# Kernel tuning notes

Measured on AMD Instinct MI355X. Metric: run time of the kernel, lower is better.

## Reference

```python
import jax, jax.numpy as jnp
import numpy as np


def setup_inputs() -> dict:
    key = jax.random.key(0)
    ks = jax.random.split(key, 8)
    T, B, I, H, A, R = 256, 256, 9, 1024, 4, 38
    return {
        "inputs": jax.random.normal(ks[0], (T, B, I), dtype=jnp.float32),
        "hidden0": jax.random.normal(ks[1], (B, H), dtype=jnp.float32),
        "actions": jax.random.normal(ks[2], (T, B, A), dtype=jnp.float32),
        "reward": jax.random.normal(ks[3], (B, R), dtype=jnp.float32),
        # parameters, initialized with the same scales as the torch module
        "i2h": jax.random.normal(ks[4], (I, H), dtype=jnp.float32) * float(10 * np.sqrt(2.0 / (I + H))),
        "h2h": jax.random.normal(ks[5], (H, H), dtype=jnp.float32) * float(np.sqrt(2.0 / H)),
        "a2h": jax.random.normal(ks[6], (A, H), dtype=jnp.float32) * float(np.sqrt(2.0 / (H + A))),
        "r2h": jax.random.normal(ks[7], (R, H), dtype=jnp.float32) * float(0.1 * np.sqrt(2.0 / (H + R))),
        "bh": jnp.zeros((1, H), dtype=jnp.float32),
        "r": 0.5 * jnp.ones((1, H), dtype=jnp.float32),  # inertia
        "k_action": 1,
    }


def reference(inputs, hidden0, actions, reward, i2h, h2h, a2h, r2h, bh, r, k_action):
    # reward @ r2h + bh is constant across timesteps -> hoist out of the scan
    rbias = reward @ r2h + bh  # [B, H]

    def step(hidden, xs):
        inp_t, act_t = xs  # [B, I], [B, A]
        h_cand = jnp.tanh(inp_t @ i2h + hidden @ h2h + k_action * (act_t @ a2h) + rbias)
        hidden = (1 - r) * h_cand + r * hidden  # leaky state blend
        return hidden, hidden

    _, hiddens = jax.lax.scan(step, hidden0, (inputs, actions))
    return hiddens  # [T, B, H] == list of hiddens in forward_sequence
```

## Files before the change

kernel.cpp:

```cpp
#include <hip/hip_runtime.h>
#include <stdint.h>
#include <math.h>

#define TT 256
#define BB 256
#define II 9
#define HH 1024
#define AAx 4
#define RR 38
#define BH (BB*HH)
#define NJB 16

typedef __attribute__((ext_vector_type(8))) short short8;
typedef __attribute__((ext_vector_type(4))) float f32x4;
typedef __attribute__((ext_vector_type(4))) unsigned int u32x4;

__device__ __forceinline__ float bf2f(unsigned short u){
  union{unsigned int i; float f;} v; v.i = ((unsigned int)u)<<16; return v.f;
}
__device__ __forceinline__ unsigned short f2bf(float f){
  union{float f; unsigned int i;} v; v.f = f;
  unsigned int r = (v.i + 0x7FFFu + ((v.i>>16)&1u)) >> 16;
  return (unsigned short)r;
}

#define ISSUE2(d0,d1,s0,s1)                                                   \
  asm volatile("global_load_dwordx4 %0, %2, off offset:" s0 " sc0 sc1\n\t"    \
               "global_load_dwordx4 %1, %2, off offset:" s1 " sc0 sc1"        \
               : "=&v"(d0), "=&v"(d1) : "v"(ap) : "memory")

#define WAITP(n,q0,q1)                                                        \
  asm volatile("s_waitcnt vmcnt(" n ")" : "+v"(q0), "+v"(q1) :: "memory")

#define STORE_CC(p,x)                                                         \
  asm volatile("global_store_dword %0, %1, off sc0 sc1" :: "v"(p), "v"(x) : "memory")

#define CVTPK(d,s0,s1)                                                        \
  asm("v_cvt_pk_bf16_f32 %0, %1, %2" : "=v"(d) : "v"(s0), "v"(s1))

__global__ __launch_bounds__(512, 2) void rnn_persist(
    const float* __restrict__ inp,  const float* __restrict__ hid0,
    const float* __restrict__ act,  const float* __restrict__ rew,
    const float* __restrict__ i2h,  const float* __restrict__ h2h,
    const float* __restrict__ a2h,  const float* __restrict__ r2h,
    const float* __restrict__ bh,   const float* __restrict__ rr,
    const int*   __restrict__ kact_p,
    float* __restrict__ out, int* __restrict__ cnt)
{
  __shared__ f32x4 part[8*4*64];
  __shared__ unsigned short sexth[16*32];
  __shared__ unsigned short sextl[16*32];

  const int tid   = threadIdx.x;
  const int w     = tid >> 6;
  const int l     = tid & 63;
  const int row16 = l & 15;
  const int quad  = l >> 4;
  const int g     = blockIdx.x & 15;
  const int jb    = blockIdx.x >> 4;

  const float kact = (float)kact_p[0];

  short8 wbh[4][4], wbl[4][4];
  #pragma unroll
  for (int ki=0; ki<4; ki++){
    const int kb = w*128 + ki*32 + quad*8;
    #pragma unroll
    for (int nt=0; nt<4; nt++){
      const int n = jb*64 + nt*16 + row16;
      short8 vh, vl;
      #pragma unroll
      for (int j=0; j<8; j++){
        const float bv = h2h[(size_t)(kb+j)*HH + n];
        const unsigned short hh = f2bf(bv);
        vh[j] = (short)hh;
        vl[j] = (short)f2bf(bv - bf2f(hh));
      }
      wbh[ki][nt] = vh; wbl[ki][nt] = vl;
    }
  }
  short8 webh[4], webl[4];
  #pragma unroll
  for (int nt=0; nt<4; nt++){
    short8 vh, vl;
    #pragma unroll
    for (int j=0; j<8; j++){
      const int k = quad*8 + j;
      const int n = jb*64 + nt*16 + row16;
      float bv = 0.f;
      if (w == 0){
        if (k < II)          bv = i2h[(size_t)k*HH + n];
        else if (k < II+AAx) bv = kact * a2h[(size_t)(k-II)*HH + n];
      }
      const unsigned short hh = f2bf(bv);
      vh[j] = (short)hh;
      vl[j] = (short)f2bf(bv - bf2f(hh));
    }
    webh[nt] = vh; webl[nt] = vl;
  }

  const int ecol = jb*64 + w*16 + row16;
  float r_own = 0.f, romr = 0.f;
  float h_own[4] = {0,0,0,0}, rb[4] = {0,0,0,0};
  if (w < 4){
    r_own = rr[ecol];
    romr  = 1.f - r_own;
    #pragma unroll
    for (int i=0; i<4; i++){
      const int br = 16*g + 4*quad + i;
      h_own[i] = hid0[(size_t)br*HH + ecol];
      float s = bh[ecol];
      for (int q=0; q<RR; q++) s += rew[(size_t)br*RR + q] * r2h[(size_t)q*HH + ecol];
      rb[i] = s;
    }
  }

  sexth[tid] = 0; sextl[tid] = 0;
  const int st_act = (tid < 16*13);
  const int st_row = st_act ? (tid / 13) : 0;
  const int st_q   = st_act ? (tid % 13) : 0;
  __syncthreads();

  float xv_cur = 0.f, xv_nxt = 0.f;
  if (st_act){
    const int br = 16*g + st_row;
    xv_cur = (st_q < II) ? inp[(size_t)br*II + st_q]
                         : act[(size_t)br*AAx + (st_q - II)];
  }

  const int arow = 16*g + row16;

  for (int t=0; t<TT; t++){
    if (st_act){
      const unsigned short hh = f2bf(xv_cur);
      sexth[st_row*32 + st_q] = hh;
      sextl[st_row*32 + st_q] = f2bf(xv_cur - bf2f(hh));
    }
    __syncthreads();

    const float* __restrict__ hp = t ? (out + (size_t)(t-1)*BH) : hid0;
    const float* ap = hp + (size_t)arow*HH + (size_t)w*128 + quad*8;

    f32x4 acc[4];
    #pragma unroll
    for (int nt=0; nt<4; nt++){ acc[nt].x=0.f; acc[nt].y=0.f; acc[nt].z=0.f; acc[nt].w=0.f; }

    auto doKi = [&](int ki, const f32x4& q0, const f32x4& q1){
      u32x4 ahw, alw;
      CVTPK(ahw[0], q0[0], q0[1]);
      CVTPK(ahw[1], q0[2], q0[3]);
      CVTPK(ahw[2], q1[0], q1[1]);
      CVTPK(ahw[3], q1[2], q1[3]);
      const float l0 = q0[0] - __builtin_bit_cast(float, ahw[0] << 16);
      const float l1 = q0[1] - __builtin_bit_cast(float, ahw[0] & 0xFFFF0000u);
      const float l2 = q0[2] - __builtin_bit_cast(float, ahw[1] << 16);
      const float l3 = q0[3] - __builtin_bit_cast(float, ahw[1] & 0xFFFF0000u);
      const float l4 = q1[0] - __builtin_bit_cast(float, ahw[2] << 16);
      const float l5 = q1[1] - __builtin_bit_cast(float, ahw[2] & 0xFFFF0000u);
      const float l6 = q1[2] - __builtin_bit_cast(float, ahw[3] << 16);
      const float l7 = q1[3] - __builtin_bit_cast(float, ahw[3] & 0xFFFF0000u);
      CVTPK(alw[0], l0, l1);
      CVTPK(alw[1], l2, l3);
      CVTPK(alw[2], l4, l5);
      CVTPK(alw[3], l6, l7);
      const short8 ah = __builtin_bit_cast(short8, ahw);
      const short8 al = __builtin_bit_cast(short8, alw);
      #pragma unroll
      for (int nt=0; nt<4; nt++){
        acc[nt] = __builtin_amdgcn_mfma_f32_16x16x32_bf16(ah, wbh[ki][nt], acc[nt], 0,0,0);
        acc[nt] = __builtin_amdgcn_mfma_f32_16x16x32_bf16(al, wbh[ki][nt], acc[nt], 0,0,0);
        acc[nt] = __builtin_amdgcn_mfma_f32_16x16x32_bf16(ah, wbl[ki][nt], acc[nt], 0,0,0);
      }
    };

    {
      f32x4 p0,p1,q0,q1;
      ISSUE2(p0,p1,"0","16");
      ISSUE2(q0,q1,"128","144");
      WAITP("2",p0,p1);
      doKi(0,p0,p1);
      ISSUE2(p0,p1,"256","272");
      WAITP("2",q0,q1);
      doKi(1,q0,q1);
      ISSUE2(q0,q1,"384","400");
      {
        const int tt2 = (t+1 < TT) ? (t+1) : (TT-1);
        const int br  = 16*g + st_row;
        const float* xp = st_act
          ? ((st_q < II) ? inp + ((size_t)tt2*BB + br)*II  + st_q
                         : act + ((size_t)tt2*BB + br)*AAx + (st_q - II))
          : inp;
        xv_nxt = *xp;
      }
      WAITP("3",p0,p1);
      doKi(2,p0,p1);
      WAITP("1",q0,q1);
      doKi(3,q0,q1);
    }

    if (w == 0){
      const short8 aeh = *(const short8*)&sexth[row16*32 + quad*8];
      const short8 ael = *(const short8*)&sextl[row16*32 + quad*8];
      #pragma unroll
      for (int nt=0; nt<4; nt++){
        acc[nt] = __builtin_amdgcn_mfma_f32_16x16x32_bf16(aeh, webh[nt], acc[nt], 0,0,0);
        acc[nt] = __builtin_amdgcn_mfma_f32_16x16x32_bf16(ael, webh[nt], acc[nt], 0,0,0);
        acc[nt] = __builtin_amdgcn_mfma_f32_16x16x32_bf16(aeh, webl[nt], acc[nt], 0,0,0);
      }
    }

    #pragma unroll
    for (int nt=0; nt<4; nt++) part[(w*4 + nt)*64 + l] = acc[nt];
    __syncthreads();

    if (w < 4){
      f32x4 z = part[(0*4 + w)*64 + l];
      #pragma unroll
      for (int s=1; s<8; s++){
        const f32x4 p = part[(s*4 + w)*64 + l];
        z.x += p.x; z.y += p.y; z.z += p.z; z.w += p.w;
      }
      const float zz[4] = {z.x, z.y, z.z, z.w};
      #pragma unroll
      for (int i=0; i<4; i++){
        const float x  = zz[i] + rb[i];
        const float hc = tanhf(x);
        const float hn = romr*hc + r_own*h_own[i];
        h_own[i] = hn;
        const int br = 16*g + 4*quad + i;
        float* op = out + (size_t)t*BH + (size_t)br*HH + ecol;
        STORE_CC(op, hn);
      }
    }

    asm volatile("s_waitcnt vmcnt(0)" ::: "memory");
    __syncthreads();
    if (tid == 0){
      __hip_atomic_fetch_add(&cnt[g*32], 1, __ATOMIC_RELAXED, __HIP_MEMORY_SCOPE_AGENT);
      const int target = NJB*(t+1);
      while (__hip_atomic_load(&cnt[g*32], __ATOMIC_RELAXED, __HIP_MEMORY_SCOPE_AGENT) < target)
        __builtin_amdgcn_s_sleep(1);
    }
    __syncthreads();

    xv_cur = xv_nxt;
  }
}

extern "C" void kernel_launch(void* const* d_in, const int* in_sizes, int n_in,
                              void* d_out, int out_size, void* d_ws, size_t ws_size,
                              hipStream_t stream) {
  const float* inp  = (const float*)d_in[0];
  const float* hid0 = (const float*)d_in[1];
  const float* act  = (const float*)d_in[2];
  const float* rew  = (const float*)d_in[3];
  const float* i2h  = (const float*)d_in[4];
  const float* h2h  = (const float*)d_in[5];
  const float* a2h  = (const float*)d_in[6];
  const float* r2h  = (const float*)d_in[7];
  const float* bh   = (const float*)d_in[8];
  const float* rr   = (const float*)d_in[9];
  const int*   kact = (const int*)d_in[10];
  float* out = (float*)d_out;

  int* cnt = (int*)d_ws;
  hipMemsetAsync(d_ws, 0, 4096, stream);

  rnn_persist<<<256, 512, 0, stream>>>(inp, hid0, act, rew, i2h, h2h, a2h, r2h,
                                       bh, rr, kact, out, cnt);
}
```

Before: 1.259 ms.

## Replace group atomic-counter barrier with per-block flags and per-wave polling

```diff
diff --git a/kernel.cpp b/kernel.cpp
--- a/kernel.cpp
+++ b/kernel.cpp
@@ -14,6 +14,7 @@
 typedef __attribute__((ext_vector_type(8))) short short8;
 typedef __attribute__((ext_vector_type(4))) float f32x4;
 typedef __attribute__((ext_vector_type(4))) unsigned int u32x4;
+typedef __attribute__((ext_vector_type(2))) unsigned int u32x2;
 
 __device__ __forceinline__ float bf2f(unsigned short u){
   union{unsigned int i; float f;} v; v.i = ((unsigned int)u)<<16; return v.f;
@@ -50,6 +51,9 @@
   __shared__ f32x4 part[8*4*64];
   __shared__ unsigned short sexth[16*32];
   __shared__ unsigned short sextl[16*32];
+  __shared__ short8 sweh[4*64];
+  __shared__ short8 swel[4*64];
+  __shared__ int done4[2];
 
   const int tid   = threadIdx.x;
   const int w     = tid >> 6;
@@ -79,24 +83,23 @@
       wbh[ki][nt] = vh; wbl[ki][nt] = vl;
     }
   }
-  short8 webh[4], webl[4];
-  #pragma unroll
-  for (int nt=0; nt<4; nt++){
-    short8 vh, vl;
-    #pragma unroll
-    for (int j=0; j<8; j++){
-      const int k = quad*8 + j;
-      const int n = jb*64 + nt*16 + row16;
-      float bv = 0.f;
-      if (w == 0){
+  if (w == 0){
+    #pragma unroll
+    for (int nt=0; nt<4; nt++){
+      short8 vh, vl;
+      #pragma unroll
+      for (int j=0; j<8; j++){
+        const int k = quad*8 + j;
+        const int n = jb*64 + nt*16 + row16;
+        float bv = 0.f;
         if (k < II)          bv = i2h[(size_t)k*HH + n];
         else if (k < II+AAx) bv = kact * a2h[(size_t)(k-II)*HH + n];
-      }
-      const unsigned short hh = f2bf(bv);
-      vh[j] = (short)hh;
-      vl[j] = (short)f2bf(bv - bf2f(hh));
-    }
-    webh[nt] = vh; webl[nt] = vl;
+        const unsigned short hh = f2bf(bv);
+        vh[j] = (short)hh;
+        vl[j] = (short)f2bf(bv - bf2f(hh));
+      }
+      sweh[nt*64 + l] = vh; swel[nt*64 + l] = vl;
+    }
   }
 
   const int ecol = jb*64 + w*16 + row16;
@@ -116,30 +119,42 @@
   }
 
   sexth[tid] = 0; sextl[tid] = 0;
+  if (tid < 2) done4[tid] = 0;
   const int st_act = (tid < 16*13);
   const int st_row = st_act ? (tid / 13) : 0;
   const int st_q   = st_act ? (tid % 13) : 0;
   __syncthreads();
 
-  float xv_cur = 0.f, xv_nxt = 0.f;
-  if (st_act){
+  const int arow = 16*g + row16;
+  unsigned* flown = (unsigned*)((char*)cnt + 1024 + (size_t)g*64 + (size_t)jb*4);
+  const unsigned* fp = (const unsigned*)((char*)cnt + 1024 + (size_t)g*64 + (size_t)w*8);
+
+  float xvr;
+  f32x4 L0a,L0b,L1a,L1b,L2a,L2b,L3a,L3b;
+  u32x2 fpre;
+  {
     const int br = 16*g + st_row;
-    xv_cur = (st_q < II) ? inp[(size_t)br*II + st_q]
-                         : act[(size_t)br*AAx + (st_q - II)];
-  }
-
-  const int arow = 16*g + row16;
+    const float* xp0 = st_act
+      ? ((st_q < II) ? inp + (size_t)br*II + st_q
+                     : act + (size_t)br*AAx + (st_q - II))
+      : inp;
+    asm volatile("global_load_dword %0, %1, off" : "=&v"(xvr) : "v"(xp0) : "memory");
+    const float* ap = hid0 + (size_t)arow*HH + (size_t)w*128 + quad*8;
+    ISSUE2(L0a,L0b,"0","16");
+    ISSUE2(L1a,L1b,"128","144");
+    ISSUE2(L2a,L2b,"256","272");
+    ISSUE2(L3a,L3b,"384","400");
+  }
 
   for (int t=0; t<TT; t++){
+    asm volatile("s_waitcnt vmcnt(8)" : "+v"(xvr) :: "memory");
     if (st_act){
-      const unsigned short hh = f2bf(xv_cur);
+      const unsigned short hh = f2bf(xvr);
       sexth[st_row*32 + st_q] = hh;
-      sextl[st_row*32 + st_q] = f2bf(xv_cur - bf2f(hh));
-    }
-    __syncthreads();
-
-    const float* __restrict__ hp = t ? (out + (size_t)(t-1)*BH) : hid0;
-    const float* ap = hp + (size_t)arow*HH + (size_t)w*128 + quad*8;
+      sextl[st_row*32 + st_q] = f2bf(xvr - bf2f(hh));
+    }
+    asm volatile("s_waitcnt lgkmcnt(0)" ::: "memory");
+    __builtin_amdgcn_s_barrier();
 
     f32x4 acc[4];
     #pragma unroll
@@ -173,45 +188,32 @@
       }
     };
 
-    {
-      f32x4 p0,p1,q0,q1;
-      ISSUE2(p0,p1,"0","16");
-      ISSUE2(q0,q1,"128","144");
-      WAITP("2",p0,p1);
-      doKi(0,p0,p1);
-      ISSUE2(p0,p1,"256","272");
-      WAITP("2",q0,q1);
-      doKi(1,q0,q1);
-      ISSUE2(q0,q1,"384","400");
-      {
-        const int tt2 = (t+1 < TT) ? (t+1) : (TT-1);
-        const int br  = 16*g + st_row;
-        const float* xp = st_act
-          ? ((st_q < II) ? inp + ((size_t)tt2*BB + br)*II  + st_q
-                         : act + ((size_t)tt2*BB + br)*AAx + (st_q - II))
-          : inp;
-        xv_nxt = *xp;
-      }
-      WAITP("3",p0,p1);
-      doKi(2,p0,p1);
-      WAITP("1",q0,q1);
-      doKi(3,q0,q1);
-    }
+    WAITP("6",L0a,L0b); doKi(0,L0a,L0b);
+    WAITP("4",L1a,L1b); doKi(1,L1a,L1b);
+    WAITP("2",L2a,L2b); doKi(2,L2a,L2b);
+    WAITP("0",L3a,L3b); doKi(3,L3a,L3b);
 
     if (w == 0){
       const short8 aeh = *(const short8*)&sexth[row16*32 + quad*8];
       const short8 ael = *(const short8*)&sextl[row16*32 + quad*8];
       #pragma unroll
       for (int nt=0; nt<4; nt++){
-        acc[nt] = __builtin_amdgcn_mfma_f32_16x16x32_bf16(aeh, webh[nt], acc[nt], 0,0,0);
-        acc[nt] = __builtin_amdgcn_mfma_f32_16x16x32_bf16(ael, webh[nt], acc[nt], 0,0,0);
-        acc[nt] = __builtin_amdgcn_mfma_f32_16x16x32_bf16(aeh, webl[nt], acc[nt], 0,0,0);
+        const short8 bh8 = sweh[nt*64 + l];
+        const short8 bl8 = swel[nt*64 + l];
+        acc[nt] = __builtin_amdgcn_mfma_f32_16x16x32_bf16(aeh, bh8, acc[nt], 0,0,0);
+        acc[nt] = __builtin_amdgcn_mfma_f32_16x16x32_bf16(ael, bh8, acc[nt], 0,0,0);
+        acc[nt] = __builtin_amdgcn_mfma_f32_16x16x32_bf16(aeh, bl8, acc[nt], 0,0,0);
       }
     }
 
     #pragma unroll
     for (int nt=0; nt<4; nt++) part[(w*4 + nt)*64 + l] = acc[nt];
-    __syncthreads();
+    if (t+1 < TT){
+      asm volatile("global_load_dwordx2 %0, %1, off sc0 sc1"
+                   : "=&v"(fpre) : "v"(fp) : "memory");
+    }
+    asm volatile("s_waitcnt lgkmcnt(0)" ::: "memory");
+    __builtin_amdgcn_s_barrier();
 
     if (w < 4){
       f32x4 z = part[(0*4 + w)*64 + l];
@@ -231,19 +233,48 @@
         float* op = out + (size_t)t*BH + (size_t)br*HH + ecol;
         STORE_CC(op, hn);
       }
-    }
-
-    asm volatile("s_waitcnt vmcnt(0)" ::: "memory");
-    __syncthreads();
-    if (tid == 0){
-      __hip_atomic_fetch_add(&cnt[g*32], 1, __ATOMIC_RELAXED, __HIP_MEMORY_SCOPE_AGENT);
-      const int target = NJB*(t+1);
-      while (__hip_atomic_load(&cnt[g*32], __ATOMIC_RELAXED, __HIP_MEMORY_SCOPE_AGENT) < target)
-        __builtin_amdgcn_s_sleep(1);
-    }
-    __syncthreads();
-
-    xv_cur = xv_nxt;
+      asm volatile("s_waitcnt vmcnt(0)" ::: "memory");
+      if (l == 0){
+        const int old = __hip_atomic_fetch_add(&done4[t&1], 1,
+                          __ATOMIC_RELAXED, __HIP_MEMORY_SCOPE_WORKGROUP);
+        if (old == 3){
+          const unsigned fvv = (unsigned)(t+1);
+          asm volatile("global_store_dword %0, %1, off sc0 sc1"
+                       :: "v"(flown), "v"(fvv) : "memory");
+          asm volatile("s_waitcnt vmcnt(0)" ::: "memory");
+          __hip_atomic_store(&done4[t&1], 0, __ATOMIC_RELAXED,
+                             __HIP_MEMORY_SCOPE_WORKGROUP);
+        }
+      }
+    }
+
+    if (t+1 < TT){
+      const unsigned tgt = (unsigned)(t+1);
+      asm volatile("s_waitcnt vmcnt(0)" : "+v"(fpre) :: "memory");
+      if (!(fpre[0] >= tgt && fpre[1] >= tgt)){
+        if (l == 0){
+          u32x2 fv;
+          for (int it=0; it<(1<<16); ++it){
+            asm volatile("global_load_dwordx2 %0, %1, off sc0 sc1\n\t"
+                         "s_waitcnt vmcnt(0)"
+                         : "=&v"(fv) : "v"(fp) : "memory");
+            if (fv[0] >= tgt && fv[1] >= tgt) break;
+            __builtin_amdgcn_s_sleep(1);
+          }
+        }
+      }
+      const int br = 16*g + st_row;
+      const float* xpn = st_act
+        ? ((st_q < II) ? inp + ((size_t)(t+1)*BB + br)*II  + st_q
+                       : act + ((size_t)(t+1)*BB + br)*AAx + (st_q - II))
+        : inp;
+      asm volatile("global_load_dword %0, %1, off" : "=&v"(xvr) : "v"(xpn) : "memory");
+      const float* ap = out + (size_t)t*BH + (size_t)arow*HH + (size_t)w*128 + quad*8;
+      ISSUE2(L0a,L0b,"0","16");
+      ISSUE2(L1a,L1b,"128","144");
+      ISSUE2(L2a,L2b,"256","272");
+      ISSUE2(L3a,L3b,"384","400");
+    }
   }
 }
 
```

Result: slower. 1.790 ms (+42.2%).
